# Kernel optimization log

Measured on AMD Instinct MI355X. Metric: run time of the kernel, lower is better.

## Reference

```python
import jax, jax.numpy as jnp
import numpy as np

EPS = 1e-8  # `eps` is an undefined global in the original repo snippet; standard capsule eps
CH_J, N_J, R_NUM = 32, 4, 3


def _squash(s):
    # Faithful to the source: norm / (1 + norm^2 + eps) * s, norm over last dim (size 1 here)
    norm = jnp.sqrt(jnp.sum(s * s, axis=-1, keepdims=True))
    return norm / (1.0 + norm ** 2 + EPS) * s


def _unif_act_wt_entropy(k):
    # k: (b, W, W, 1, ch_j, ch_i); softmax was taken over (W, W, ch_j) per (b, ch_i).
    # Entropy of coupling coefficients normalized by uniform entropy, averaged.
    b, ci = k.shape[0], k.shape[-1]
    p = jnp.transpose(k, (0, 5, 3, 1, 2, 4)).reshape(b, ci, -1)
    ent = -jnp.sum(p * jnp.log(p + EPS), axis=-1)
    return jnp.mean(ent / jnp.log(jnp.asarray(p.shape[-1], p.dtype)))


def reference(inputs, conv_w, conv_b):
    b, ch_i, n_i, h, w = inputs.shape
    # (b, 1, ch_i*n_i, h, w) -> Conv3d stride (n_i,1,1), pad (0,1,1)
    x = inputs.reshape(b, 1, ch_i * n_i, h, w)
    x = jax.lax.conv_general_dilated(
        x, conv_w, window_strides=(n_i, 1, 1),
        padding=((0, 0), (1, 1), (1, 1)),
        dimension_numbers=('NCDHW', 'OIDHW', 'NCDHW'))
    x = x + conv_b[None, :, None, None, None]
    W = x.shape[-1]
    # (b, ch_i, ch_j*n_j, W, W) -> (b, W, W, n_j, ch_j, ch_i)
    x = jnp.transpose(x, (0, 2, 1, 3, 4)).reshape(b, ch_i, CH_J, N_J, W, W)
    x = jnp.transpose(x, (0, 4, 5, 3, 2, 1))

    B = jnp.zeros((b, W, W, 1, CH_J, ch_i), dtype=x.dtype)
    S_hat = None
    k = None
    for i in range(R_NUM):
        # softmax over (W, W, ch_j) jointly, per (b, ch_i)
        logits = jnp.transpose(B, (0, 5, 3, 1, 2, 4)).reshape(b, ch_i, 1, -1)
        k = jax.nn.softmax(logits, axis=-1)
        k = jnp.transpose(k.reshape(b, ch_i, 1, W, W, CH_J), (0, 3, 4, 2, 5, 1))
        S = jnp.sum(k * x, axis=-1, keepdims=True)  # (b, W, W, n_j, ch_j, 1)
        S_hat = _squash(S)
        if i < R_NUM - 1:
            B = B + jnp.sum(S_hat * x, axis=3, keepdims=True)

    out = jnp.transpose(S_hat[..., 0], (0, 4, 3, 1, 2))  # (b, ch_j, n_j, W, W)
    return out, _unif_act_wt_entropy(k)


def setup_inputs() -> dict:
    key = jax.random.key(0)
    k1, k2, k3 = jax.random.split(key, 3)
    inputs = jax.random.normal(k1, (8, 32, 8, 32, 32), dtype=jnp.float32)
    conv_w = jax.random.normal(k2, (128, 1, 3, 3, 3), dtype=jnp.float32) * 0.05
    conv_b = jax.random.normal(k3, (128,), dtype=jnp.float32) * 0.05
    return {"inputs": inputs, "conv_w": conv_w, "conv_b": conv_b}
```

## Files before the change

### kernel.cpp

```cpp
#include <hip/hip_runtime.h>
#include <hip/hip_bf16.h>

#define EPSF 1e-8f

typedef short bf16x8 __attribute__((ext_vector_type(8)));
typedef float f32x4 __attribute__((ext_vector_type(4)));


__device__ __forceinline__ float bflo(unsigned u){ return __uint_as_float(u<<16); }
__device__ __forceinline__ float bfhi(unsigned u){ return __uint_as_float(u&0xffff0000u); }
__device__ __forceinline__ float bfu16(unsigned short u){ return __uint_as_float((unsigned)u<<16); }
__device__ __forceinline__ unsigned bfpack2(float a,float b){
    return (__float_as_uint(a)>>16)|(__float_as_uint(b)&0xffff0000u);
}
__device__ __forceinline__ unsigned short bfr16(float a){
    return (unsigned short)(__float_as_uint(a)>>16);
}
__device__ __forceinline__ float fastrcp(float x){ return __builtin_amdgcn_rcpf(x); }
__device__ __forceinline__ bf16x8 pack8(const float* v){
    union { unsigned u[4]; bf16x8 v8; } cv;
#pragma unroll
    for (int j = 0; j < 4; ++j) cv.u[j] = bfpack2(v[2*j], v[2*j+1]);
    return cv.v8;
}

template<int PHASE>
__global__ __launch_bounds__(256, 6) void k_caps(
    const float* __restrict__ in, const float* __restrict__ cw,
    unsigned short* __restrict__ wg,
    const float* __restrict__ cb, unsigned* __restrict__ Bpk,
    const float* __restrict__ sm_in, const float* __restrict__ siz_in,
    float* __restrict__ pm, float* __restrict__ ps, float* __restrict__ pt,
    float* __restrict__ outp) {
    __shared__ __align__(16) unsigned char smem[25728];
    unsigned short* slabB = (unsigned short*)smem;
    unsigned short* wLT = (unsigned short*)(smem + 4608);
    float* cbL  = (float*)(smem + 12032);
    float* smL  = (float*)(smem + 12544);
    float* sizL = (float*)(smem + 12672);
    unsigned* ktab = (unsigned*)(smem + 12800);

    const int t = threadIdx.x;
    const int lane = t & 63, wid = t >> 6;
    const int bid = blockIdx.x;
    const int bh = bid >> 3, b = bh >> 5, h = bh & 31;
    const int w0 = (bid & 7) << 2;
    const int l15 = lane & 15, lq = lane >> 4;

    unsigned char* wb = smem + 12928 + (size_t)wid * 3200;
    unsigned* Bu  = (unsigned*)wb;
    float* shL    = (float*)(wb + 2560);
    float* auxL   = (float*)(wb + 3072);
    float* statb  = (float*)(wb + 2560);

    for (int j = t; j < 864; j += 256) {
        const int r = j / 3, q = j - r * 3;
        const int ci2 = r / 9, rem = r - ci2 * 9, kd = rem / 3, dy = rem - kd * 3;
        const int y = h + dy - 1;
        const int x0 = w0 - 4 + q * 4;
        float4 f = {0.f, 0.f, 0.f, 0.f};
        if ((unsigned)y < 32u && (unsigned)x0 < 32u)
            f = *reinterpret_cast<const float4*>(
                in + (((size_t)(b * 32 + ci2) * 8 + kd) * 32 + y) * 32 + x0);
        unsigned* sp = (unsigned*)slabB + r * 4;
        if (q == 0)      sp[0] = bfpack2(f.z, f.w);
        else if (q == 1) { sp[1] = bfpack2(f.x, f.y);
                           sp[2] = bfpack2(f.z, f.w); }
        else             sp[3] = bfpack2(f.x, f.y);
    }
    if constexpr (PHASE == 0) {
        for (int j = t; j < 3456; j += 256) {
            const int c = j / 27, k = j - c * 27;
            wLT[k * 132 + c] = bfr16(cw[j]);
        }
    } else {
        const uint4* wg4 = (const uint4*)wg;
        uint4* wl4 = (uint4*)wLT;
        for (int j = t; j < 464; j += 256) wl4[j] = wg4[j];
    }
    if (t < 128) cbL[t] = cb[t];
    if (t < 32) {
        const int k = t < 27 ? t : 26;
        const int kd = k / 9, r9 = k - kd * 9, dy = r9 / 3, dx = r9 - dy * 3;
        ktab[t] = (unsigned)((kd * 3 + dy) * 8 + dx);
    }
    if constexpr (PHASE >= 1) {
        if (t < 32) { smL[t] = sm_in[b * 32 + t]; sizL[t] = siz_in[b * 32 + t]; }
    }
    __syncthreads();

    if constexpr (PHASE == 0) {
        if (bid == 0) {
            const uint4* wl4 = (const uint4*)wLT;
            uint4* wg4 = (uint4*)wg;
            for (int j = t; j < 464; j += 256) wg4[j] = wl4[j];
        }
    }

    const size_t loc = (size_t)bh * 32 + w0 + wid;
    const int tb = wid + 1;

    float b1v[16];
    if constexpr (PHASE == 0) {
        const int k2 = lane >> 1, half = lane & 1;
        float vs = 0.f;
        if (k2 < 27) {
            const unsigned short* sp = slabB + half * 16 * 72 + ktab[k2] + tb;
#pragma unroll
            for (int i = 0; i < 16; ++i) vs += bfu16(sp[i * 72]);
        }
        vs += __shfl_xor(vs, 1);
        if (half == 0 && k2 < 27) auxL[k2] = vs;
    } else {
        const uint4* Bg = (const uint4*)(Bpk + loc * 512 + (size_t)lane * 8);
        const uint4 q0 = Bg[0], q1 = Bg[1];
        const unsigned pk[8] = {q0.x, q0.y, q0.z, q0.w, q1.x, q1.y, q1.z, q1.w};
#pragma unroll
        for (int e = 0; e < 8; ++e) { b1v[2*e] = bflo(pk[e]); b1v[2*e+1] = bfhi(pk[e]); }
#pragma unroll
        for (int mt = 0; mt < 2; ++mt)
#pragma unroll
        for (int reg = 0; reg < 4; ++reg)
#pragma unroll
        for (int nt = 0; nt < 2; ++nt) {
            const float me = b1v[mt*8 + nt*4 + reg];
            const float ot = __shfl_xor(me, 1);
            const unsigned pku = (l15 & 1) ? bfpack2(ot, me) : bfpack2(me, ot);
            if ((l15 & 1) == nt)
                Bu[(mt*16 + lq*4 + reg)*20 + nt*8 + (l15 >> 1)] = pku;
        }
        bf16x8 kmA[2];
#pragma unroll
        for (int mt = 0; mt < 2; ++mt) {
            const uint4 q = *(const uint4*)(Bu + (mt*16 + l15)*20 + lq*4);
            const unsigned uu[4] = {q.x, q.y, q.z, q.w};
            float ev[8];
#pragma unroll
            for (int j2 = 0; j2 < 4; ++j2) {
                const int ci0 = lq*8 + 2*j2;
                ev[2*j2]   = __expf(bflo(uu[j2]) - smL[ci0])   * sizL[ci0];
                ev[2*j2+1] = __expf(bfhi(uu[j2]) - smL[ci0+1]) * sizL[ci0+1];
            }
            kmA[mt] = pack8(ev);
        }
        bf16x8 vtB[2];
#pragma unroll
        for (int nt = 0; nt < 2; ++nt) {
            const int kt = nt*16 + l15;
            const unsigned ko = ktab[kt];
            union { unsigned short s[8]; bf16x8 v8; } cv;
#pragma unroll
            for (int j = 0; j < 8; ++j) {
                const unsigned short sv = slabB[(lq*8 + j)*72 + ko + tb];
                cv.s[j] = (kt < 27) ? sv : (unsigned short)(kt == 27 ? 0x3f80 : 0);
            }
            vtB[nt] = cv.v8;
        }
        f32x4 accu[2][2];
#pragma unroll
        for (int mt = 0; mt < 2; ++mt)
#pragma unroll
        for (int nt = 0; nt < 2; ++nt)
            accu[mt][nt] = __builtin_amdgcn_mfma_f32_16x16x32_bf16(
                kmA[mt], vtB[nt], (f32x4){0.f,0.f,0.f,0.f}, 0, 0, 0);
#pragma unroll
        for (int mt = 0; mt < 2; ++mt)
#pragma unroll
        for (int reg = 0; reg < 4; ++reg)
#pragma unroll
        for (int nt = 0; nt < 2; ++nt) {
            const float me = accu[mt][nt][reg];
            const float ot = __shfl_xor(me, 1);
            const unsigned pku = (l15 & 1) ? bfpack2(ot, me) : bfpack2(me, ot);
            if ((l15 & 1) == nt)
                Bu[(mt*16 + lq*4 + reg)*20 + nt*8 + (l15 >> 1)] = pku;
        }
    }

#pragma unroll
    for (int cc = 0; cc < 2; ++cc) {
        const int c = lane + cc * 64;
        float S;
        if constexpr (PHASE == 0) {
            S = 0.f;
#pragma unroll
            for (int k = 0; k < 27; ++k)
                S = fmaf(bfu16(wLT[k*132 + c]), auxL[k], S);
            S = S * (1.0f/32768.0f) + cbL[c] * (1.0f/1024.0f);
        } else {
            const unsigned* up = Bu + (c >> 2) * 20;
            S = 0.f;
#pragma unroll
            for (int p = 0; p < 13; ++p) {
                const unsigned u = up[p];
                S = fmaf(bfu16(wLT[(2*p)*132 + c]),   bflo(u), S);
                S = fmaf(bfu16(wLT[(2*p+1)*132 + c]), bfhi(u), S);
            }
            const unsigned u13 = up[13];
            S = fmaf(bfu16(wLT[26*132 + c]), bflo(u13), S);
            S = fmaf(cbL[c], bfhi(u13), S);
        }
        const float sq = fabsf(S) * S * fastrcp(1.f + S*S + EPSF);
        shL[c] = sq;
    }

    if constexpr (PHASE == 2) {
        __syncthreads();
        if (t < 128) {
            const float* s0 = (const float*)(smem + 12928 + 0*3200 + 2560);
            const float* s1 = (const float*)(smem + 12928 + 1*3200 + 2560);
            const float* s2 = (const float*)(smem + 12928 + 2*3200 + 2560);
            const float* s3 = (const float*)(smem + 12928 + 3*3200 + 2560);
            float4 o = make_float4(s0[t], s1[t], s2[t], s3[t]);
            *reinterpret_cast<float4*>(
                outp + ((size_t)(b*128 + t))*1024 + (size_t)h*32 + w0) = o;
        }
        if (bid == 0) {
            float* er = (float*)smem;
            er[t] = pt[t];
            __syncthreads();
            for (int s2v = 128; s2v > 0; s2v >>= 1) {
                if (t < s2v) er[t] += er[t + s2v];
                __syncthreads();
            }
            if (t == 0) outp[1048576] = er[0] * (1.0f/256.0f);
        }
        return;
    }

    {
        const int k0 = 2*l15, k1 = k0 + 1;
#pragma unroll
        for (int i = 0; i < 8; ++i) {
            const int cj = lq + 4*i;
            float v0 = 0.f, v1 = 0.f;
            if (k0 < 27) {
#pragma unroll
                for (int nj = 0; nj < 4; ++nj)
                    v0 = fmaf(shL[cj*4+nj], bfu16(wLT[k0*132 + cj*4 + nj]), v0);
            }
            if (k1 < 27) {
#pragma unroll
                for (int nj = 0; nj < 4; ++nj)
                    v1 = fmaf(shL[cj*4+nj], bfu16(wLT[k1*132 + cj*4 + nj]), v1);
            }
            Bu[cj*20 + l15] = bfpack2(v0, v1);
        }
        if (lane < 32) {
            float cv = 0.f;
#pragma unroll
            for (int nj = 0; nj < 4; ++nj)
                cv = fmaf(shL[lane*4+nj], cbL[lane*4+nj], cv);
            auxL[lane] = cv;
        }
    }

    bf16x8 wsA[2], vB[2];
#pragma unroll
    for (int mt = 0; mt < 2; ++mt) {
        union { uint4 q4; bf16x8 v8; } cv;
        cv.q4 = *(const uint4*)(Bu + (mt*16 + l15)*20 + lq*4);
        wsA[mt] = cv.v8;
    }
#pragma unroll
    for (int nt = 0; nt < 2; ++nt) {
        const int ci = nt*16 + l15;
        union { unsigned short s[8]; bf16x8 v8; } cv;
#pragma unroll
        for (int j = 0; j < 8; ++j) {
            const int k = lq*8 + j;
            const unsigned short sv = slabB[ci*72 + ktab[k] + tb];
            cv.s[j] = (k < 27) ? sv : (unsigned short)0;
        }
        vB[nt] = cv.v8;
    }
    f32x4 accb[2][2];
#pragma unroll
    for (int mt = 0; mt < 2; ++mt)
#pragma unroll
    for (int nt = 0; nt < 2; ++nt)
        accb[mt][nt] = __builtin_amdgcn_mfma_f32_16x16x32_bf16(
            wsA[mt], vB[nt], (f32x4){0.f,0.f,0.f,0.f}, 0, 0, 0);

    float bnew[16];
#pragma unroll
    for (int mt = 0; mt < 2; ++mt)
#pragma unroll
    for (int nt = 0; nt < 2; ++nt)
#pragma unroll
    for (int reg = 0; reg < 4; ++reg) {
        float val = accb[mt][nt][reg] + auxL[mt*16 + lq*4 + reg];
        if constexpr (PHASE == 1) val += b1v[mt*8 + nt*4 + reg];
        bnew[mt*8 + nt*4 + reg] = val;
    }
    {
        unsigned pk[8];
#pragma unroll
        for (int e = 0; e < 8; ++e) pk[e] = bfpack2(bnew[2*e], bnew[2*e+1]);
        uint4* Bg = (uint4*)(Bpk + loc * 512 + (size_t)lane * 8);
        Bg[0] = make_uint4(pk[0], pk[1], pk[2], pk[3]);
        Bg[1] = make_uint4(pk[4], pk[5], pk[6], pk[7]);
    }
    float m2[2], s2[2], T2[2];
#pragma unroll
    for (int nt = 0; nt < 2; ++nt) {
        float m = -1e30f;
#pragma unroll
        for (int mt = 0; mt < 2; ++mt)
#pragma unroll
        for (int reg = 0; reg < 4; ++reg) m = fmaxf(m, bnew[mt*8 + nt*4 + reg]);
        float s = 0.f, T = 0.f;
#pragma unroll
        for (int mt = 0; mt < 2; ++mt)
#pragma unroll
        for (int reg = 0; reg < 4; ++reg) {
            const float d = bnew[mt*8 + nt*4 + reg] - m;
            const float e = __expf(d);
            s += e; T += e * d;
        }
        m2[nt] = m; s2[nt] = s; T2[nt] = T;
#pragma unroll
        for (int off = 16; off <= 32; off <<= 1) {
            const float mo = __shfl_xor(m2[nt], off);
            const float so = __shfl_xor(s2[nt], off);
            const float To = __shfl_xor(T2[nt], off);
            const float nm = fmaxf(m2[nt], mo);
            const float ea = __expf(m2[nt]-nm), eb = __expf(mo-nm);
            T2[nt] = ea*(T2[nt] + s2[nt]*(m2[nt]-nm)) + eb*(To + so*(mo-nm));
            s2[nt] = ea*s2[nt] + eb*so;
            m2[nt] = nm;
        }
    }
    if (lane < 16) {
#pragma unroll
        for (int nt = 0; nt < 2; ++nt) {
            const int ci = nt*16 + lane;
            statb[ci] = m2[nt]; statb[32+ci] = s2[nt]; statb[64+ci] = T2[nt];
        }
    }
    __syncthreads();
    if (t < 32) {
        float M = -1e30f, Z = 0.f, T = 0.f;
#pragma unroll
        for (int wv = 0; wv < 4; ++wv) {
            const float* sw = (const float*)(smem + 12928 + wv*3200 + 2560);
            const float mo = sw[t], so = sw[32+t], To = sw[64+t];
            const float nm = fmaxf(M, mo);
            const float ea = __expf(M-nm), eb = __expf(mo-nm);
            T = ea*(T + Z*(M-nm)) + eb*(To + so*(mo-nm));
            Z = ea*Z + eb*so;
            M = nm;
        }
        pm[bid*32 + t] = M;
        ps[bid*32 + t] = Z;
        if constexpr (PHASE == 1) pt[bid*32 + t] = T;
    }
}

template <int NPART, bool ENT>
__global__ __launch_bounds__(256) void k_comb(const float* __restrict__ pm,
                                              const float* __restrict__ ps,
                                              const float* __restrict__ pt,
                                              float* __restrict__ sm,
                                              float* __restrict__ siz,
                                              float* __restrict__ entp) {
    const int b = blockIdx.x, t = threadIdx.x;
    const int ci = t & 31, seg = t >> 5;
    constexpr int PER = NPART / 8;
    __shared__ float red[3][8][33];

    float M = -1e30f;
    for (int k = 0; k < PER; ++k)
        M = fmaxf(M, pm[((size_t)b * NPART + seg * PER + k) * 32 + ci]);
    red[0][seg][ci] = M;
    __syncthreads();
    float Mg = red[0][0][ci];
#pragma unroll
    for (int q = 1; q < 8; ++q) Mg = fmaxf(Mg, red[0][q][ci]);

    float Z = 0.0f, T = 0.0f;
    for (int k = 0; k < PER; ++k) {
        const size_t i = ((size_t)b * NPART + seg * PER + k) * 32 + ci;
        const float dm = pm[i] - Mg;
        const float e = __expf(dm);
        Z += ps[i] * e;
        if constexpr (ENT) T += (pt[i] + ps[i] * dm) * e;
    }
    red[1][seg][ci] = Z;
    if constexpr (ENT) red[2][seg][ci] = T;
    __syncthreads();
    if (t < 32) {
        float Zt = 0.0f, Tt = 0.0f;
#pragma unroll
        for (int q = 0; q < 8; ++q) {
            Zt += red[1][q][ci];
            if constexpr (ENT) Tt += red[2][q][ci];
        }
        sm[b * 32 + ci] = Mg;
        siz[b * 32 + ci] = 1.0f / Zt;
        if constexpr (ENT)
            entp[b * 32 + ci] = (logf(Zt) - Tt / Zt) * (1.0f / 10.39720770839918f);
    }
}

extern "C" void kernel_launch(void* const* d_in, const int* in_sizes, int n_in,
                              void* d_out, int out_size, void* d_ws, size_t ws_size,
                              hipStream_t stream) {
    const float* in = (const float*)d_in[0];
    const float* cw = (const float*)d_in[1];
    const float* cb = (const float*)d_in[2];
    float* out = (float*)d_out;

    unsigned* Bpk = (unsigned*)d_ws;
    float* pm0  = (float*)(Bpk + 4194304);
    float* ps0  = pm0 + 65536;
    float* pm1  = ps0 + 65536;
    float* ps1  = pm1 + 65536;
    float* pt1  = ps1 + 65536;
    float* sm0  = pt1 + 65536;
    float* siz0 = sm0 + 256;
    float* sm1  = siz0 + 256;
    float* siz1 = sm1 + 256;
    float* entp = siz1 + 256;
    unsigned short* wg = (unsigned short*)(entp + 256);

    k_caps<0><<<2048, 256, 0, stream>>>(in, cw, wg, cb, Bpk,
                                        nullptr, nullptr, pm0, ps0, pt1, out);
    k_comb<256, false><<<8, 256, 0, stream>>>(pm0, ps0, nullptr, sm0, siz0, nullptr);
    k_caps<1><<<2048, 256, 0, stream>>>(in, cw, wg, cb, Bpk,
                                        sm0, siz0, pm1, ps1, pt1, out);
    k_comb<256, true><<<8, 256, 0, stream>>>(pm1, ps1, pt1, sm1, siz1, entp);
    k_caps<2><<<2048, 256, 0, stream>>>(in, cw, wg, cb, Bpk,
                                        sm1, siz1, pm1, ps1, entp, out);
}
```

Before: 81.30 us.

## Replace per-block partial stats and combine kernels with atomic global softmax sums

```diff
diff --git a/kernel.cpp b/kernel.cpp
--- a/kernel.cpp
+++ b/kernel.cpp
@@ -29,8 +29,8 @@
     const float* __restrict__ in, const float* __restrict__ cw,
     unsigned short* __restrict__ wg,
     const float* __restrict__ cb, unsigned* __restrict__ Bpk,
-    const float* __restrict__ sm_in, const float* __restrict__ siz_in,
-    float* __restrict__ pm, float* __restrict__ ps, float* __restrict__ pt,
+    const float* __restrict__ zin, float* __restrict__ zout,
+    float* __restrict__ tout,
     float* __restrict__ outp) {
     __shared__ __align__(16) unsigned char smem[25728];
     unsigned short* slabB = (unsigned short*)smem;
@@ -85,7 +85,7 @@
         ktab[t] = (unsigned)((kd * 3 + dy) * 8 + dx);
     }
     if constexpr (PHASE >= 1) {
-        if (t < 32) { smL[t] = sm_in[b * 32 + t]; sizL[t] = siz_in[b * 32 + t]; }
+        if (t < 32) { smL[t] = 0.f; sizL[t] = 1.0f / zin[b * 32 + t]; }
     }
     __syncthreads();
 
@@ -217,7 +217,9 @@
         }
         if (bid == 0) {
             float* er = (float*)smem;
-            er[t] = pt[t];
+            const float Zv = zin[t];
+            const float Tv = tout[t];
+            er[t] = (logf(Zv) - Tv / Zv) * (1.0f/10.39720770839918f);
             __syncthreads();
             for (int s2v = 128; s2v > 0; s2v >>= 1) {
                 if (t < s2v) er[t] += er[t + s2v];
@@ -351,55 +353,10 @@
             Z = ea*Z + eb*so;
             M = nm;
         }
-        pm[bid*32 + t] = M;
-        ps[bid*32 + t] = Z;
-        if constexpr (PHASE == 1) pt[bid*32 + t] = T;
-    }
-}
-
-template <int NPART, bool ENT>
-__global__ __launch_bounds__(256) void k_comb(const float* __restrict__ pm,
-                                              const float* __restrict__ ps,
-                                              const float* __restrict__ pt,
-                                              float* __restrict__ sm,
-                                              float* __restrict__ siz,
-                                              float* __restrict__ entp) {
-    const int b = blockIdx.x, t = threadIdx.x;
-    const int ci = t & 31, seg = t >> 5;
-    constexpr int PER = NPART / 8;
-    __shared__ float red[3][8][33];
-
-    float M = -1e30f;
-    for (int k = 0; k < PER; ++k)
-        M = fmaxf(M, pm[((size_t)b * NPART + seg * PER + k) * 32 + ci]);
-    red[0][seg][ci] = M;
-    __syncthreads();
-    float Mg = red[0][0][ci];
-#pragma unroll
-    for (int q = 1; q < 8; ++q) Mg = fmaxf(Mg, red[0][q][ci]);
-
-    float Z = 0.0f, T = 0.0f;
-    for (int k = 0; k < PER; ++k) {
-        const size_t i = ((size_t)b * NPART + seg * PER + k) * 32 + ci;
-        const float dm = pm[i] - Mg;
-        const float e = __expf(dm);
-        Z += ps[i] * e;
-        if constexpr (ENT) T += (pt[i] + ps[i] * dm) * e;
-    }
-    red[1][seg][ci] = Z;
-    if constexpr (ENT) red[2][seg][ci] = T;
-    __syncthreads();
-    if (t < 32) {
-        float Zt = 0.0f, Tt = 0.0f;
-#pragma unroll
-        for (int q = 0; q < 8; ++q) {
-            Zt += red[1][q][ci];
-            if constexpr (ENT) Tt += red[2][q][ci];
-        }
-        sm[b * 32 + ci] = Mg;
-        siz[b * 32 + ci] = 1.0f / Zt;
-        if constexpr (ENT)
-            entp[b * 32 + ci] = (logf(Zt) - Tt / Zt) * (1.0f / 10.39720770839918f);
+        const float em = __expf(M);
+        atomicAdd(&zout[b*32 + t], Z * em);
+        if constexpr (PHASE == 1)
+            atomicAdd(&tout[b*32 + t], em * (T + Z * M));
     }
 }
 
@@ -412,24 +369,16 @@
     float* out = (float*)d_out;
 
     unsigned* Bpk = (unsigned*)d_ws;
-    float* pm0  = (float*)(Bpk + 4194304);
-    float* ps0  = pm0 + 65536;
-    float* pm1  = ps0 + 65536;
-    float* ps1  = pm1 + 65536;
-    float* pt1  = ps1 + 65536;
-    float* sm0  = pt1 + 65536;
-    float* siz0 = sm0 + 256;
-    float* sm1  = siz0 + 256;
-    float* siz1 = sm1 + 256;
-    float* entp = siz1 + 256;
-    unsigned short* wg = (unsigned short*)(entp + 256);
-
+    float* Z0 = (float*)(Bpk + 4194304);
+    float* Z1 = Z0 + 256;
+    float* T1 = Z1 + 256;
+    unsigned short* wg = (unsigned short*)(T1 + 256);
+
+    hipMemsetAsync(Z0, 0, 3 * 256 * sizeof(float), stream);
     k_caps<0><<<2048, 256, 0, stream>>>(in, cw, wg, cb, Bpk,
-                                        nullptr, nullptr, pm0, ps0, pt1, out);
-    k_comb<256, false><<<8, 256, 0, stream>>>(pm0, ps0, nullptr, sm0, siz0, nullptr);
+                                        nullptr, Z0, nullptr, out);
     k_caps<1><<<2048, 256, 0, stream>>>(in, cw, wg, cb, Bpk,
-                                        sm0, siz0, pm1, ps1, pt1, out);
-    k_comb<256, true><<<8, 256, 0, stream>>>(pm1, ps1, pt1, sm1, siz1, entp);
+                                        Z0, Z1, T1, out);
     k_caps<2><<<2048, 256, 0, stream>>>(in, cw, wg, cb, Bpk,
-                                        sm1, siz1, pm1, ps1, entp, out);
-}
+                                        Z1, nullptr, T1, out);
+}
```

Result: slower. 92.41 us (+13.7%).
